# Optimization experiments

Hardware: AMD Instinct MI355X
Metric: run time of the kernel (lower is better)

## Reference

```python
import jax, jax.numpy as jnp
import numpy as np

N_EMBD = 2048
N_HEAD = 16
KV_GROUP = 4
HEAD_DIM = N_EMBD // N_HEAD          # 128
N_KV = N_HEAD // KV_GROUP            # 4
KV_DIM = N_KV * HEAD_DIM             # 512
B, T = 2, 2048
ROPE_THETA = 1000000.0


def setup_inputs() -> dict:
    key = jax.random.key(0)
    k0, k1, k2 = jax.random.split(key, 3)
    x = jax.random.normal(k0, (B, T, N_EMBD), dtype=jnp.float32)
    # weights stored (in, out); matches torch Linear math up to a transpose of random init
    W_attn = jax.random.normal(k1, (N_EMBD, N_EMBD + 2 * KV_DIM), dtype=jnp.float32) * 0.02
    b_attn = jnp.zeros((N_EMBD + 2 * KV_DIM,), dtype=jnp.float32)
    W_proj = jax.random.normal(k2, (N_EMBD, N_EMBD), dtype=jnp.float32) * 0.02
    # realistic RoPE frequencies (Qwen-style theta)
    inv_freq = 1.0 / (ROPE_THETA ** (np.arange(0, HEAD_DIM, 2, dtype=np.float64) / HEAD_DIM))
    ang = np.outer(np.arange(T, dtype=np.float64), inv_freq)  # (T, HEAD_DIM//2)
    freqs_cos = jnp.asarray(np.cos(ang), dtype=jnp.float32)
    freqs_sin = jnp.asarray(np.sin(ang), dtype=jnp.float32)
    return {"x": x, "W_attn": W_attn, "b_attn": b_attn, "W_proj": W_proj,
            "freqs_cos": freqs_cos, "freqs_sin": freqs_sin}


def _rope_expand(x, cos, sin, kv_group):
    # x: (B, T, n_kv, hd); complex rotate interleaved pairs, then expand to n_kv*kv_group heads
    Bx, Tx, nh, hd = x.shape
    xf = x.astype(jnp.float32).reshape(Bx, Tx, nh, hd // 2, 2)
    a, b = xf[..., 0], xf[..., 1]
    c = cos[None, :, None, :]  # (1, T, 1, hd//2)
    s = sin[None, :, None, :]
    yr = a * c - b * s
    yi = a * s + b * c
    y = jnp.stack([yr, yi], axis=-1).reshape(Bx, Tx, nh, hd)
    y = jnp.broadcast_to(y[:, :, :, None, :], (Bx, Tx, nh, kv_group, hd))
    return y.reshape(Bx, Tx, nh * kv_group, hd).astype(x.dtype)


def reference(x, W_attn, b_attn, W_proj, freqs_cos, freqs_sin):
    Bx, Tx, E = x.shape
    hd = 2 * freqs_cos.shape[-1]
    n_q = E // hd
    kv_dim = (W_attn.shape[1] - E) // 2
    n_kv = kv_dim // hd
    g = n_q // n_kv

    qkv = x @ W_attn + b_attn  # (B, T, E + 2*kv_dim)
    q = qkv[..., :E].reshape(Bx, Tx, n_q, hd).transpose(0, 2, 1, 3)          # bhtd
    k = qkv[..., E:E + kv_dim].reshape(Bx, Tx, n_kv, hd)
    v = qkv[..., E + kv_dim:].reshape(Bx, Tx, n_kv, hd)
    # faithful to source: RoPE on K AND V (not Q), then GQA expand
    k = _rope_expand(k, freqs_cos, freqs_sin, g).transpose(0, 2, 1, 3)       # bhtd
    v = _rope_expand(v, freqs_cos, freqs_sin, g).transpose(0, 2, 1, 3)       # bhtd

    scale = 1.0 / jnp.sqrt(jnp.asarray(hd, dtype=x.dtype))
    scores = jnp.einsum('bhqd,bhkd->bhqk', q, k) * scale                     # (B, H, T, T)
    causal = jnp.tril(jnp.ones((Tx, Tx), dtype=bool))
    scores = jnp.where(causal, scores, jnp.asarray(-jnp.inf, scores.dtype))
    attn = jax.nn.softmax(scores, axis=-1)
    y = jnp.einsum('bhqk,bhkd->bhqd', attn, v)
    y = y.transpose(0, 2, 1, 3).reshape(Bx, Tx, E)
    return y @ W_proj  # c_proj, no bias
```

## Files before the change

kernel.cpp:

```cpp
#include <hip/hip_runtime.h>
#include <cstdint>
#include <cstddef>

#define T_SEQ 2048
#define B_SZ  2
#define EMB   2048
#define NH    16
#define NKV   4
#define HD    128
#define KVD   512
#define QKVN  3072
#define MROWS (B_SZ*T_SEQ)

typedef __bf16 bf16x8 __attribute__((ext_vector_type(8)));
typedef float  f32x4  __attribute__((ext_vector_type(4)));
typedef short  s16x8  __attribute__((ext_vector_type(8)));
typedef unsigned short u16;

__device__ __forceinline__ u16 f2b(float f) {
  uint32_t u = __builtin_bit_cast(uint32_t, f);
  u += 0x7fffu + ((u >> 16) & 1u);
  return (u16)(u >> 16);
}
__device__ __forceinline__ float b2f(u16 h) {
  return __builtin_bit_cast(float, (uint32_t)h << 16);
}
__device__ __forceinline__ bf16x8 ld_bf8(const u16* p) {
  return __builtin_bit_cast(bf16x8, *(const s16x8*)p);
}
__device__ __forceinline__ void glds16(const void* g, void* l) {
  __builtin_amdgcn_global_load_lds((const __attribute__((address_space(1))) void*)g,
                                   (__attribute__((address_space(3))) void*)l, 16, 0, 0);
}

__global__ void cvt_x_kernel(const float4* __restrict__ x, ushort4* __restrict__ xb, int n4) {
  int i = blockIdx.x*blockDim.x + threadIdx.x;
  if (i >= n4) return;
  float4 v = x[i];
  ushort4 o;
  o.x = f2b(v.x); o.y = f2b(v.y); o.z = f2b(v.z); o.w = f2b(v.w);
  xb[i] = o;
}

__global__ void transpose_w_kernel(const float* __restrict__ in, u16* __restrict__ out,
                                   int R, int C) {
  __shared__ float tile[32][33];
  int c0 = blockIdx.x*32, r0 = blockIdx.y*32;
  int tx = threadIdx.x, ty = threadIdx.y;
#pragma unroll
  for (int i = 0; i < 32; i += 8)
    tile[ty+i][tx] = in[(size_t)(r0+ty+i)*C + c0+tx];
  __syncthreads();
#pragma unroll
  for (int i = 0; i < 32; i += 8)
    out[(size_t)(c0+ty+i)*R + r0+tx] = f2b(tile[tx][ty+i]);
}

template<bool BF16_OUT>
__global__ __launch_bounds__(256) void gemm_kernel(const u16* __restrict__ A,
        const u16* __restrict__ Bt, const float* __restrict__ bias,
        void* __restrict__ Cout, int M, int N, int K) {
  __shared__ u16 As[128*64];
  __shared__ u16 Bs[128*64];
  const int tid = threadIdx.x;
  const int w = tid >> 6, lane = tid & 63;
  const int quad = lane >> 4, lc = lane & 15;
  const int m0 = blockIdx.y*128, n0 = blockIdx.x*128;
  const int wm = (w >> 1)*64, wn = (w & 1)*64;
  f32x4 acc[4][4] = {};
  int xoff[2];
#pragma unroll
  for (int ks = 0; ks < 2; ++ks) xoff[ks] = ((ks*4 + quad) ^ (lc & 7))*8;
  int srow[4], spos[4];
#pragma unroll
  for (int r = 0; r < 4; ++r) {
    int c = r*256 + tid;
    srow[r] = c >> 3;
    spos[r] = ((c & 7) ^ (srow[r] & 7))*8;
  }
  for (int k0 = 0; k0 < K; k0 += 64) {
    __syncthreads();
#pragma unroll
    for (int r = 0; r < 4; ++r) {
      glds16(A  + (size_t)(m0+srow[r])*K + k0 + spos[r], As + (size_t)(r*256 + w*64)*8);
      glds16(Bt + (size_t)(n0+srow[r])*K + k0 + spos[r], Bs + (size_t)(r*256 + w*64)*8);
    }
    __syncthreads();
#pragma unroll
    for (int ks = 0; ks < 2; ++ks) {
      bf16x8 af[4], bfr[4];
#pragma unroll
      for (int i = 0; i < 4; ++i) af[i]  = ld_bf8(As + (wm + i*16 + lc)*64 + xoff[ks]);
#pragma unroll
      for (int j = 0; j < 4; ++j) bfr[j] = ld_bf8(Bs + (wn + j*16 + lc)*64 + xoff[ks]);
#pragma unroll
      for (int i = 0; i < 4; ++i)
#pragma unroll
        for (int j = 0; j < 4; ++j)
          acc[i][j] = __builtin_amdgcn_mfma_f32_16x16x32_bf16(af[i], bfr[j], acc[i][j], 0, 0, 0);
    }
  }
#pragma unroll
  for (int j = 0; j < 4; ++j) {
    int col = n0 + wn + j*16 + lc;
    float bv = BF16_OUT ? bias[col] : 0.0f;
#pragma unroll
    for (int i = 0; i < 4; ++i) {
      int rowb = m0 + wm + i*16 + quad*4;
#pragma unroll
      for (int r = 0; r < 4; ++r) {
        float v = acc[i][j][r] + bv;
        if (BF16_OUT) ((u16*)Cout)[(size_t)(rowb+r)*N + col] = f2b(v);
        else          ((float*)Cout)[(size_t)(rowb+r)*N + col] = v;
      }
    }
  }
}

__global__ void rope_kernel(const u16* __restrict__ qkv, const float* __restrict__ fc,
                            const float* __restrict__ fs, u16* __restrict__ kout,
                            u16* __restrict__ vout) {
  int tid = threadIdx.x;
  int row = blockIdx.x;
  int i = tid & 63, kv = tid >> 6;
  int t = row & (T_SEQ-1);
  const u16* p = qkv + (size_t)row*QKVN + EMB + kv*HD + 2*i;
  float ka = b2f(p[0]),   kb = b2f(p[1]);
  float va = b2f(p[KVD]), vb = b2f(p[KVD+1]);
  float c = fc[t*64+i], s = fs[t*64+i];
  size_t ob = (size_t)row*KVD + kv*HD + 2*i;
  kout[ob]   = f2b(ka*c - kb*s);
  kout[ob+1] = f2b(ka*s + kb*c);
  vout[ob]   = f2b(va*c - vb*s);
  vout[ob+1] = f2b(va*s + vb*c);
}

__global__ void transpose_v_kernel(const u16* __restrict__ vb, u16* __restrict__ vtb) {
  __shared__ u16 tile[32][33];
  int bkv = blockIdx.z;
  int b = bkv >> 2, kv = bkv & 3;
  int d0 = blockIdx.y*32, t0 = blockIdx.x*32;
  int tx = threadIdx.x, ty = threadIdx.y;
#pragma unroll
  for (int i = 0; i < 32; i += 8)
    tile[ty+i][tx] = vb[(size_t)(b*T_SEQ + t0+ty+i)*KVD + kv*HD + d0 + tx];
  __syncthreads();
#pragma unroll
  for (int i = 0; i < 32; i += 8)
    vtb[(size_t)(bkv*HD + d0+ty+i)*T_SEQ + t0 + tx] = tile[tx][ty+i];
}

__global__ __launch_bounds__(256, 3) void flash_kernel(const u16* __restrict__ qkv,
    const u16* __restrict__ kb, const u16* __restrict__ vtb, u16* __restrict__ yb) {
  constexpr int PP = 72;
  __shared__ u16 Ks[64*128];
  __shared__ u16 Vs[128*64];
  __shared__ u16 Ps[4][16*PP];
  const int tid = threadIdx.x;
  const int w = tid >> 6, lane = tid & 63;
  const int quad = lane >> 4, lc = lane & 15;
  const int bkv = blockIdx.x & 7;
  const int r_  = blockIdx.x >> 3;
  const int b = bkv >> 2, kv = bkv & 3;
  const int h = kv*4 + w;
  const int qbase = (127 - r_)*16;

  bf16x8 qf[4];
  {
    const u16* qp = qkv + (size_t)(b*T_SEQ + qbase + lc)*QKVN + h*HD + quad*8;
#pragma unroll
    for (int ks = 0; ks < 4; ++ks) qf[ks] = ld_bf8(qp + ks*32);
  }

  f32x4 o[8] = {};
  float rs[4] = {0.f, 0.f, 0.f, 0.f};
  const u16* kbase = kb  + (size_t)b*T_SEQ*KVD + kv*HD;
  const u16* vbase = vtb + (size_t)bkv*HD*T_SEQ;
  const int nk = qbase + 16;
  const float cs = 0.08838834764831845f * 1.4426950408889634f;
  u16* pw = Ps[w];

  int koff[4], voff[2];
#pragma unroll
  for (int ks = 0; ks < 4; ++ks) koff[ks] = lc*128 + (((ks*4 + quad) ^ lc)*8);
#pragma unroll
  for (int ks = 0; ks < 2; ++ks) voff[ks] = lc*64 + (((ks*4 + quad) ^ (lc & 7))*8);

  for (int k0 = 0; k0 < nk; k0 += 64) {
    __syncthreads();
#pragma unroll
    for (int rr = 0; rr < 4; ++rr) {
      int krow = (rr*4 + w)*4 + (lane >> 4);
      int ccg  = (lane & 15) ^ (krow & 15);
      glds16(kbase + (size_t)(k0 + krow)*KVD + ccg*8, Ks + (size_t)(rr*4 + w)*512);
    }
#pragma unroll
    for (int rr = 0; rr < 4; ++rr) {
      int vrow = (rr*4 + w)*8 + (lane >> 3);
      int ccg  = (lane & 7) ^ (vrow & 7);
      glds16(vbase + (size_t)vrow*T_SEQ + k0 + ccg*8, Vs + (size_t)(rr*4 + w)*512);
    }
    __syncthreads();

    f32x4 sc[4] = {};
#pragma unroll
    for (int nt = 0; nt < 4; ++nt)
#pragma unroll
      for (int ks = 0; ks < 4; ++ks) {
        bf16x8 kf = ld_bf8(Ks + nt*16*128 + koff[ks]);
        sc[nt] = __builtin_amdgcn_mfma_f32_16x16x32_bf16(qf[ks], kf, sc[nt], 0, 0, 0);
      }

    if (k0 + 63 > qbase) {
#pragma unroll
      for (int nt = 0; nt < 4; ++nt) {
        int key = k0 + nt*16 + lc;
        int qrow = qbase + quad*4;
#pragma unroll
        for (int r = 0; r < 4; ++r) {
          float p = (key <= qrow + r) ? exp2f(sc[nt][r]*cs) : 0.0f;
          rs[r] += p;
          pw[(quad*4 + r)*PP + nt*16 + lc] = f2b(p);
        }
      }
    } else {
#pragma unroll
      for (int nt = 0; nt < 4; ++nt)
#pragma unroll
        for (int r = 0; r < 4; ++r) {
          float p = exp2f(sc[nt][r]*cs);
          rs[r] += p;
          pw[(quad*4 + r)*PP + nt*16 + lc] = f2b(p);
        }
    }

    bf16x8 pa[2];
#pragma unroll
    for (int ks = 0; ks < 2; ++ks)
      pa[ks] = ld_bf8(pw + lc*PP + ks*32 + quad*8);

#pragma unroll
    for (int j = 0; j < 8; ++j)
#pragma unroll
      for (int ks = 0; ks < 2; ++ks) {
        bf16x8 vf = ld_bf8(Vs + j*16*64 + voff[ks]);
        o[j] = __builtin_amdgcn_mfma_f32_16x16x32_bf16(pa[ks], vf, o[j], 0, 0, 0);
      }
  }

#pragma unroll
  for (int r = 0; r < 4; ++r) {
    float v = rs[r];
#pragma unroll
    for (int off2 = 8; off2 >= 1; off2 >>= 1)
      v += __shfl_xor(v, off2);
    float inv = 1.0f / v;
    size_t orow = (size_t)(b*T_SEQ + qbase + quad*4 + r)*EMB + h*HD;
#pragma unroll
    for (int j = 0; j < 8; ++j)
      yb[orow + j*16 + lc] = f2b(o[j][r]*inv);
  }
}

extern "C" void kernel_launch(void* const* d_in, const int* in_sizes, int n_in,
                              void* d_out, int out_size, void* d_ws, size_t ws_size,
                              hipStream_t stream) {
  const float* x      = (const float*)d_in[0];
  const float* W_attn = (const float*)d_in[1];
  const float* b_attn = (const float*)d_in[2];
  const float* W_proj = (const float*)d_in[3];
  const float* fc     = (const float*)d_in[4];
  const float* fs     = (const float*)d_in[5];

  u16* ws   = (u16*)d_ws;
  u16* xb   = ws;
  u16* WaT  = xb   + (size_t)MROWS*EMB;
  u16* qkv  = WaT  + (size_t)QKVN*EMB;
  u16* kbuf = qkv  + (size_t)MROWS*QKVN;
  u16* vb   = kbuf + (size_t)MROWS*KVD;
  u16* vtb  = vb   + (size_t)MROWS*KVD;
  u16* WpT  = WaT;
  u16* yb   = xb;
  float* out = (float*)d_out;

  cvt_x_kernel<<<(MROWS*EMB/4 + 255)/256, 256, 0, stream>>>(
      (const float4*)x, (ushort4*)xb, MROWS*EMB/4);
  transpose_w_kernel<<<dim3(QKVN/32, EMB/32), dim3(32, 8), 0, stream>>>(
      W_attn, WaT, EMB, QKVN);
  gemm_kernel<true><<<dim3(QKVN/128, MROWS/128), 256, 0, stream>>>(
      xb, WaT, b_attn, qkv, MROWS, QKVN, EMB);
  rope_kernel<<<MROWS, 256, 0, stream>>>(qkv, fc, fs, kbuf, vb);
  transpose_v_kernel<<<dim3(T_SEQ/32, HD/32, B_SZ*NKV), dim3(32, 8), 0, stream>>>(vb, vtb);
  transpose_w_kernel<<<dim3(EMB/32, EMB/32), dim3(32, 8), 0, stream>>>(
      W_proj, WpT, EMB, EMB);
  flash_kernel<<<dim3(B_SZ*NKV*(T_SEQ/16)), 256, 0, stream>>>(qkv, kbuf, vtb, yb);
  gemm_kernel<false><<<dim3(EMB/128, MROWS/128), 256, 0, stream>>>(
      yb, WpT, nullptr, out, MROWS, EMB, EMB);
}
```

Measured before the change: 307.0 us.

## Replace GEMM with 256x256 double-buffered, phase-scheduled MFMA pipeline

Both projection GEMMs move to a 512-thread kernel with 256x256 output tiles and double-buffered LDS. Global-to-LDS loads of the next K tile are interleaved with MFMA phases, using explicit barriers, waitcnt and setprio scheduling. The aim is to hide memory latency and raise data reuse per block. In exchange there are far fewer blocks (192 and 128), which can leave CUs idle, and register pressure is higher.

```diff
diff --git a/kernel.cpp b/kernel.cpp
--- a/kernel.cpp
+++ b/kernel.cpp
@@ -57,56 +57,136 @@
 }
 
 template<bool BF16_OUT>
-__global__ __launch_bounds__(256) void gemm_kernel(const u16* __restrict__ A,
+__global__ __launch_bounds__(512, 2) void gemm256_kernel(const u16* __restrict__ A,
         const u16* __restrict__ Bt, const float* __restrict__ bias,
         void* __restrict__ Cout, int M, int N, int K) {
-  __shared__ u16 As[128*64];
-  __shared__ u16 Bs[128*64];
+  __shared__ u16 As[2][16384];
+  __shared__ u16 Bs[2][16384];
   const int tid = threadIdx.x;
   const int w = tid >> 6, lane = tid & 63;
   const int quad = lane >> 4, lc = lane & 15;
-  const int m0 = blockIdx.y*128, n0 = blockIdx.x*128;
-  const int wm = (w >> 1)*64, wn = (w & 1)*64;
-  f32x4 acc[4][4] = {};
-  int xoff[2];
-#pragma unroll
-  for (int ks = 0; ks < 2; ++ks) xoff[ks] = ((ks*4 + quad) ^ (lc & 7))*8;
-  int srow[4], spos[4];
-#pragma unroll
-  for (int r = 0; r < 4; ++r) {
-    int c = r*256 + tid;
-    srow[r] = c >> 3;
-    spos[r] = ((c & 7) ^ (srow[r] & 7))*8;
-  }
-  for (int k0 = 0; k0 < K; k0 += 64) {
-    __syncthreads();
-#pragma unroll
-    for (int r = 0; r < 4; ++r) {
-      glds16(A  + (size_t)(m0+srow[r])*K + k0 + spos[r], As + (size_t)(r*256 + w*64)*8);
-      glds16(Bt + (size_t)(n0+srow[r])*K + k0 + spos[r], Bs + (size_t)(r*256 + w*64)*8);
-    }
-    __syncthreads();
-#pragma unroll
-    for (int ks = 0; ks < 2; ++ks) {
-      bf16x8 af[4], bfr[4];
-#pragma unroll
-      for (int i = 0; i < 4; ++i) af[i]  = ld_bf8(As + (wm + i*16 + lc)*64 + xoff[ks]);
-#pragma unroll
-      for (int j = 0; j < 4; ++j) bfr[j] = ld_bf8(Bs + (wn + j*16 + lc)*64 + xoff[ks]);
-#pragma unroll
-      for (int i = 0; i < 4; ++i)
-#pragma unroll
-        for (int j = 0; j < 4; ++j)
-          acc[i][j] = __builtin_amdgcn_mfma_f32_16x16x32_bf16(af[i], bfr[j], acc[i][j], 0, 0, 0);
-    }
-  }
+  const int wr = w >> 2, wc = w & 3;
+  const int m0 = blockIdx.y*256, n0 = blockIdx.x*256;
+
+  f32x4 acc[8][4] = {};
+  bf16x8 af[4][2], bfv[4][2];
+
+  int aoff[2];
+#pragma unroll
+  for (int ks = 0; ks < 2; ++ks) aoff[ks] = ((ks*4 + quad) ^ (lc & 7))*8;
+  const int arow = (wr*128 + lc)*64;
+  const int brow = (wc*64  + lc)*64;
+
+  const int r0 = tid >> 3,          p0 = (tid & 7) ^ (r0 & 7);
+  const int r1 = (tid + 512) >> 3,  p1 = (tid & 7) ^ (r1 & 7);
+  const u16* sa0 = A  + (size_t)(m0 + r0)*K + p0*8;
+  const u16* sa1 = A  + (size_t)(m0 + r1)*K + p1*8;
+  const u16* sb0 = Bt + (size_t)(n0 + r0)*K + p0*8;
+  const u16* sb1 = Bt + (size_t)(n0 + r1)*K + p1*8;
+  const int wch = w*512;
+
+#define STAGE_A(bf_, h_, t_) do { \
+    glds16(sa0 + (size_t)(h_)*128*K + (t_)*64, &As[bf_][(h_)*8192 + wch]); \
+    glds16(sa1 + (size_t)(h_)*128*K + (t_)*64, &As[bf_][(h_)*8192 + 4096 + wch]); \
+  } while (0)
+#define STAGE_B(bf_, h_, t_) do { \
+    glds16(sb0 + (size_t)(h_)*128*K + (t_)*64, &Bs[bf_][(h_)*8192 + wch]); \
+    glds16(sb1 + (size_t)(h_)*128*K + (t_)*64, &Bs[bf_][(h_)*8192 + 4096 + wch]); \
+  } while (0)
+#define LDA03(S) do { _Pragma("unroll") for (int i = 0; i < 4; ++i) { \
+    af[i][0] = ld_bf8((S) + arow + i*1024 + aoff[0]); \
+    af[i][1] = ld_bf8((S) + arow + i*1024 + aoff[1]); } } while (0)
+#define LDA47(S) do { _Pragma("unroll") for (int i = 0; i < 4; ++i) { \
+    af[i][0] = ld_bf8((S) + arow + 4096 + i*1024 + aoff[0]); \
+    af[i][1] = ld_bf8((S) + arow + 4096 + i*1024 + aoff[1]); } } while (0)
+#define LDB01(S) do { _Pragma("unroll") for (int j = 0; j < 2; ++j) { \
+    bfv[j][0] = ld_bf8((S) + brow + j*1024 + aoff[0]); \
+    bfv[j][1] = ld_bf8((S) + brow + j*1024 + aoff[1]); } } while (0)
+#define LDB23(S) do { _Pragma("unroll") for (int j = 2; j < 4; ++j) { \
+    bfv[j][0] = ld_bf8((S) + brow + j*1024 + aoff[0]); \
+    bfv[j][1] = ld_bf8((S) + brow + j*1024 + aoff[1]); } } while (0)
+#define QUAD(ib_, jb_) do { _Pragma("unroll") for (int ks = 0; ks < 2; ++ks) \
+    _Pragma("unroll") for (int i = 0; i < 4; ++i) \
+    _Pragma("unroll") for (int j = 0; j < 2; ++j) \
+      acc[(ib_)+i][(jb_)+j] = __builtin_amdgcn_mfma_f32_16x16x32_bf16( \
+          af[i][ks], bfv[(jb_)+j][ks], acc[(ib_)+i][(jb_)+j], 0, 0, 0); } while (0)
+#define BARX()  __builtin_amdgcn_s_barrier()
+#define SCHB()  __builtin_amdgcn_sched_barrier(0)
+#define VMCNT(n_) do { asm volatile("s_waitcnt vmcnt(" #n_ ")" ::: "memory"); SCHB(); } while (0)
+#define MFMAPH(ib_, jb_) do { BARX(); \
+    asm volatile("s_waitcnt lgkmcnt(0)" ::: "memory"); SCHB(); \
+    __builtin_amdgcn_s_setprio(1); QUAD(ib_, jb_); __builtin_amdgcn_s_setprio(0); \
+  } while (0)
+
+  const int NT = K >> 6;
+  STAGE_A(0, 0, 0); STAGE_A(0, 1, 0); STAGE_B(0, 0, 0); STAGE_B(0, 1, 0);
+  STAGE_B(1, 0, 1); STAGE_B(1, 1, 1);
+  VMCNT(4);
+  BARX(); SCHB();
+
+  for (int t0 = 0; t0 < NT-2; t0 += 2) {
+    const int t1 = t0 + 1;
+    const u16 *a0 = As[0], *b0 = Bs[0], *a1 = As[1], *b1 = Bs[1];
+    LDA03(a0); LDB01(b0); STAGE_A(1, 0, t1);
+    MFMAPH(0, 0); BARX();
+    LDB23(b0); STAGE_A(1, 1, t1);
+    MFMAPH(0, 2); BARX();
+    LDA47(a0); STAGE_B(0, 0, t0+2);
+    MFMAPH(4, 0); BARX();
+    STAGE_B(0, 1, t0+2);
+    MFMAPH(4, 2);
+    VMCNT(4);
+    BARX(); SCHB();
+    LDA03(a1); LDB01(b1); STAGE_A(0, 0, t0+2);
+    MFMAPH(0, 0); BARX();
+    LDB23(b1); STAGE_A(0, 1, t0+2);
+    MFMAPH(0, 2); BARX();
+    LDA47(a1); STAGE_B(1, 0, t1+2);
+    MFMAPH(4, 0); BARX();
+    STAGE_B(1, 1, t1+2);
+    MFMAPH(4, 2);
+    VMCNT(4);
+    BARX(); SCHB();
+  }
+  {
+    const u16 *a0 = As[0], *b0 = Bs[0], *a1 = As[1], *b1 = Bs[1];
+    LDA03(a0); LDB01(b0); STAGE_A(1, 0, NT-1);
+    MFMAPH(0, 0); BARX();
+    LDB23(b0); STAGE_A(1, 1, NT-1);
+    MFMAPH(0, 2); BARX();
+    LDA47(a0);
+    MFMAPH(4, 0); BARX();
+    MFMAPH(4, 2);
+    VMCNT(0);
+    BARX(); SCHB();
+    LDA03(a1); LDB01(b1);
+    MFMAPH(0, 0); BARX();
+    LDB23(b1);
+    MFMAPH(0, 2); BARX();
+    LDA47(a1);
+    MFMAPH(4, 0); BARX();
+    MFMAPH(4, 2);
+  }
+
+#undef STAGE_A
+#undef STAGE_B
+#undef LDA03
+#undef LDA47
+#undef LDB01
+#undef LDB23
+#undef QUAD
+#undef BARX
+#undef SCHB
+#undef VMCNT
+#undef MFMAPH
+
 #pragma unroll
   for (int j = 0; j < 4; ++j) {
-    int col = n0 + wn + j*16 + lc;
+    int col = n0 + wc*64 + j*16 + lc;
     float bv = BF16_OUT ? bias[col] : 0.0f;
 #pragma unroll
-    for (int i = 0; i < 4; ++i) {
-      int rowb = m0 + wm + i*16 + quad*4;
+    for (int i = 0; i < 8; ++i) {
+      int rowb = m0 + wr*128 + i*16 + quad*4;
 #pragma unroll
       for (int r = 0; r < 4; ++r) {
         float v = acc[i][j][r] + bv;
@@ -287,13 +367,13 @@
       (const float4*)x, (ushort4*)xb, MROWS*EMB/4);
   transpose_w_kernel<<<dim3(QKVN/32, EMB/32), dim3(32, 8), 0, stream>>>(
       W_attn, WaT, EMB, QKVN);
-  gemm_kernel<true><<<dim3(QKVN/128, MROWS/128), 256, 0, stream>>>(
+  gemm256_kernel<true><<<dim3(QKVN/256, MROWS/256), 512, 0, stream>>>(
       xb, WaT, b_attn, qkv, MROWS, QKVN, EMB);
   rope_kernel<<<MROWS, 256, 0, stream>>>(qkv, fc, fs, kbuf, vb);
   transpose_v_kernel<<<dim3(T_SEQ/32, HD/32, B_SZ*NKV), dim3(32, 8), 0, stream>>>(vb, vtb);
   transpose_w_kernel<<<dim3(EMB/32, EMB/32), dim3(32, 8), 0, stream>>>(
       W_proj, WpT, EMB, EMB);
   flash_kernel<<<dim3(B_SZ*NKV*(T_SEQ/16)), 256, 0, stream>>>(qkv, kbuf, vtb, yb);
-  gemm_kernel<false><<<dim3(EMB/128, MROWS/128), 256, 0, stream>>>(
+  gemm256_kernel<false><<<dim3(EMB/256, MROWS/256), 512, 0, stream>>>(
       yb, WpT, nullptr, out, MROWS, EMB, EMB);
 }
```

After: 309.3 us. No clear change (+0.8%).

## Rewrite GEMM with double-buffered LDS pipeline, larger tiles, and block swizzle

Applied to the files above, without the earlier changes.

Replaces the single-buffered 128x128 GEMM with a templated 512-thread kernel that uses 256-row tiles and double-buffered LDS. Global-to-LDS loads for the next K tile are interleaved with MFMA phases under explicit vmcnt waits, barriers and setprio. A swizzled block index is also added to improve L2 reuse. In exchange it needs much more LDS and more registers, and the hand-written wait counts and barriers are fragile.

```diff
diff --git a/kernel.cpp b/kernel.cpp
--- a/kernel.cpp
+++ b/kernel.cpp
@@ -32,6 +32,12 @@
   __builtin_amdgcn_global_load_lds((const __attribute__((address_space(1))) void*)g,
                                    (__attribute__((address_space(3))) void*)l, 16, 0, 0);
 }
+template<int N> __device__ __forceinline__ void waitv() {
+  if constexpr (N == 0) asm volatile("s_waitcnt vmcnt(0)" ::: "memory");
+  else if constexpr (N == 2) asm volatile("s_waitcnt vmcnt(2)" ::: "memory");
+  else if constexpr (N == 3) asm volatile("s_waitcnt vmcnt(3)" ::: "memory");
+  __builtin_amdgcn_sched_barrier(0);
+}
 
 __global__ void cvt_x_kernel(const float4* __restrict__ x, ushort4* __restrict__ xb, int n4) {
   int i = blockIdx.x*blockDim.x + threadIdx.x;
@@ -56,57 +62,128 @@
     out[(size_t)(c0+ty+i)*R + r0+tx] = f2b(tile[tx][ty+i]);
 }
 
-template<bool BF16_OUT>
-__global__ __launch_bounds__(256) void gemm_kernel(const u16* __restrict__ A,
+template<int BN, int WGN, int MF, int NF, int NF1, int SB, int SB1, int VMC, bool BF16_OUT>
+__global__ __launch_bounds__(512, 2) void gemm_kernel(const u16* __restrict__ A,
         const u16* __restrict__ Bt, const float* __restrict__ bias,
         void* __restrict__ Cout, int M, int N, int K) {
-  __shared__ u16 As[128*64];
-  __shared__ u16 Bs[128*64];
+  constexpr int MF2 = MF/2;
+  __shared__ u16 As[2][256*64];
+  __shared__ u16 Bs[2][BN*64];
   const int tid = threadIdx.x;
   const int w = tid >> 6, lane = tid & 63;
   const int quad = lane >> 4, lc = lane & 15;
-  const int m0 = blockIdx.y*128, n0 = blockIdx.x*128;
-  const int wm = (w >> 1)*64, wn = (w & 1)*64;
-  f32x4 acc[4][4] = {};
+  const int wrow = w / WGN, wcol = w % WGN;
+  const int gx = gridDim.x;
+  const int lin = blockIdx.y*gx + blockIdx.x;
+  const int swz = (lin & 7)*32 + (lin >> 3);
+  const int m0 = (swz / gx)*256, n0 = (swz % gx)*BN;
+
+  f32x4 acc[MF][NF] = {};
+  bf16x8 af[MF2][2], bfv[NF][2];
+
   int xoff[2];
 #pragma unroll
   for (int ks = 0; ks < 2; ++ks) xoff[ks] = ((ks*4 + quad) ^ (lc & 7))*8;
-  int srow[4], spos[4];
-#pragma unroll
-  for (int r = 0; r < 4; ++r) {
-    int c = r*256 + tid;
-    srow[r] = c >> 3;
-    spos[r] = ((c & 7) ^ (srow[r] & 7))*8;
-  }
-  for (int k0 = 0; k0 < K; k0 += 64) {
-    __syncthreads();
-#pragma unroll
-    for (int r = 0; r < 4; ++r) {
-      glds16(A  + (size_t)(m0+srow[r])*K + k0 + spos[r], As + (size_t)(r*256 + w*64)*8);
-      glds16(Bt + (size_t)(n0+srow[r])*K + k0 + spos[r], Bs + (size_t)(r*256 + w*64)*8);
-    }
-    __syncthreads();
-#pragma unroll
-    for (int ks = 0; ks < 2; ++ks) {
-      bf16x8 af[4], bfr[4];
-#pragma unroll
-      for (int i = 0; i < 4; ++i) af[i]  = ld_bf8(As + (wm + i*16 + lc)*64 + xoff[ks]);
-#pragma unroll
-      for (int j = 0; j < 4; ++j) bfr[j] = ld_bf8(Bs + (wn + j*16 + lc)*64 + xoff[ks]);
-#pragma unroll
-      for (int i = 0; i < 4; ++i)
-#pragma unroll
-        for (int j = 0; j < 4; ++j)
-          acc[i][j] = __builtin_amdgcn_mfma_f32_16x16x32_bf16(af[i], bfr[j], acc[i][j], 0, 0, 0);
-    }
-  }
-#pragma unroll
-  for (int j = 0; j < 4; ++j) {
-    int col = n0 + wn + j*16 + lc;
+  const int arow0 = (wrow*MF*16 + lc)*64;
+  const int brow0 = (wcol*NF*16 + lc)*64;
+
+  const int srb  = tid >> 3;
+  const int spos = (tid & 7) ^ (srb & 7);
+  const u16* sAp = A  + (size_t)(m0 + srb)*K + spos*8;
+  const u16* sBp = Bt + (size_t)(n0 + srb)*K + spos*8;
+
+#define STAGE_A(bf_, t_, h_) do { \
+    glds16(sAp + (size_t)((h_)*2  )*64*K + (size_t)(t_)*64, &As[bf_][((h_)*2  )*4096 + w*512]); \
+    glds16(sAp + (size_t)((h_)*2+1)*64*K + (size_t)(t_)*64, &As[bf_][((h_)*2+1)*4096 + w*512]); \
+  } while (0)
+#define STAGE_B(bf_, t_, p_) do { \
+    _Pragma("unroll") for (int r = (p_) ? SB1 : 0; r < ((p_) ? SB : SB1); ++r) \
+      glds16(sBp + (size_t)r*64*K + (size_t)(t_)*64, &Bs[bf_][r*4096 + w*512]); \
+  } while (0)
+#define LDAH(S_, h_) do { _Pragma("unroll") for (int i = 0; i < MF2; ++i) { \
+    af[i][0] = ld_bf8((S_) + arow0 + ((h_)*MF2 + i)*1024 + xoff[0]); \
+    af[i][1] = ld_bf8((S_) + arow0 + ((h_)*MF2 + i)*1024 + xoff[1]); } } while (0)
+#define LDBG(S_, g_) do { _Pragma("unroll") for (int j = (g_) ? NF1 : 0; j < ((g_) ? NF : NF1); ++j) { \
+    bfv[j][0] = ld_bf8((S_) + brow0 + j*1024 + xoff[0]); \
+    bfv[j][1] = ld_bf8((S_) + brow0 + j*1024 + xoff[1]); } } while (0)
+#define CL(h_, g_) do { _Pragma("unroll") for (int ks = 0; ks < 2; ++ks) \
+    _Pragma("unroll") for (int i = 0; i < MF2; ++i) \
+    _Pragma("unroll") for (int j = (g_) ? NF1 : 0; j < ((g_) ? NF : NF1); ++j) \
+      acc[(h_)*MF2+i][j] = __builtin_amdgcn_mfma_f32_16x16x32_bf16( \
+          af[i][ks], bfv[j][ks], acc[(h_)*MF2+i][j], 0, 0, 0); } while (0)
+#define BARX()  __builtin_amdgcn_s_barrier()
+#define SCHB()  __builtin_amdgcn_sched_barrier(0)
+#define MFMAPH(h_, g_) do { BARX(); \
+    asm volatile("s_waitcnt lgkmcnt(0)" ::: "memory"); SCHB(); \
+    __builtin_amdgcn_s_setprio(1); CL(h_, g_); __builtin_amdgcn_s_setprio(0); \
+  } while (0)
+
+  const int NT = K >> 6;
+  STAGE_B(0, 0, 0); STAGE_B(0, 0, 1);
+  STAGE_A(0, 0, 0); STAGE_A(0, 0, 1);
+  STAGE_B(1, 1, 0); STAGE_B(1, 1, 1);
+  waitv<VMC>();
+  BARX(); SCHB();
+
+  for (int t0 = 0; t0 < NT-2; t0 += 2) {
+    const u16 *a0 = As[0], *b0 = Bs[0], *a1 = As[1], *b1 = Bs[1];
+    LDAH(a0, 0); LDBG(b0, 0); STAGE_A(1, t0+1, 0);
+    MFMAPH(0, 0); BARX();
+    LDBG(b0, 1); STAGE_A(1, t0+1, 1);
+    MFMAPH(0, 1); BARX();
+    LDAH(a0, 1); STAGE_B(0, t0+2, 0);
+    MFMAPH(1, 0); BARX();
+    STAGE_B(0, t0+2, 1);
+    MFMAPH(1, 1);
+    waitv<VMC>();
+    BARX(); SCHB();
+    LDAH(a1, 0); LDBG(b1, 0); STAGE_A(0, t0+2, 0);
+    MFMAPH(0, 0); BARX();
+    LDBG(b1, 1); STAGE_A(0, t0+2, 1);
+    MFMAPH(0, 1); BARX();
+    LDAH(a1, 1); STAGE_B(1, t0+3, 0);
+    MFMAPH(1, 0); BARX();
+    STAGE_B(1, t0+3, 1);
+    MFMAPH(1, 1);
+    waitv<VMC>();
+    BARX(); SCHB();
+  }
+  {
+    const u16 *a0 = As[0], *b0 = Bs[0], *a1 = As[1], *b1 = Bs[1];
+    LDAH(a0, 0); LDBG(b0, 0); STAGE_A(1, NT-1, 0);
+    MFMAPH(0, 0); BARX();
+    LDBG(b0, 1); STAGE_A(1, NT-1, 1);
+    MFMAPH(0, 1); BARX();
+    LDAH(a0, 1);
+    MFMAPH(1, 0); BARX();
+    MFMAPH(1, 1);
+    waitv<0>();
+    BARX(); SCHB();
+    LDAH(a1, 0); LDBG(b1, 0);
+    MFMAPH(0, 0); BARX();
+    LDBG(b1, 1);
+    MFMAPH(0, 1); BARX();
+    LDAH(a1, 1);
+    MFMAPH(1, 0); BARX();
+    MFMAPH(1, 1);
+  }
+
+#undef STAGE_A
+#undef STAGE_B
+#undef LDAH
+#undef LDBG
+#undef CL
+#undef BARX
+#undef SCHB
+#undef MFMAPH
+
+#pragma unroll
+  for (int j = 0; j < NF; ++j) {
+    int col = n0 + wcol*NF*16 + j*16 + lc;
     float bv = BF16_OUT ? bias[col] : 0.0f;
 #pragma unroll
-    for (int i = 0; i < 4; ++i) {
-      int rowb = m0 + wm + i*16 + quad*4;
+    for (int i = 0; i < MF; ++i) {
+      int rowb = m0 + wrow*MF*16 + i*16 + quad*4;
 #pragma unroll
       for (int r = 0; r < 4; ++r) {
         float v = acc[i][j][r] + bv;
@@ -287,13 +364,15 @@
       (const float4*)x, (ushort4*)xb, MROWS*EMB/4);
   transpose_w_kernel<<<dim3(QKVN/32, EMB/32), dim3(32, 8), 0, stream>>>(
       W_attn, WaT, EMB, QKVN);
-  gemm_kernel<true><<<dim3(QKVN/128, MROWS/128), 256, 0, stream>>>(
+  gemm_kernel<192, 4, 8, 3, 2, 3, 2, 3, true>
+      <<<dim3(QKVN/192, MROWS/256), 512, 0, stream>>>(
       xb, WaT, b_attn, qkv, MROWS, QKVN, EMB);
   rope_kernel<<<MROWS, 256, 0, stream>>>(qkv, fc, fs, kbuf, vb);
   transpose_v_kernel<<<dim3(T_SEQ/32, HD/32, B_SZ*NKV), dim3(32, 8), 0, stream>>>(vb, vtb);
   transpose_w_kernel<<<dim3(EMB/32, EMB/32), dim3(32, 8), 0, stream>>>(
       W_proj, WpT, EMB, EMB);
   flash_kernel<<<dim3(B_SZ*NKV*(T_SEQ/16)), 256, 0, stream>>>(qkv, kbuf, vtb, yb);
-  gemm_kernel<false><<<dim3(EMB/128, MROWS/128), 256, 0, stream>>>(
+  gemm_kernel<128, 2, 4, 4, 2, 2, 1, 2, false>
+      <<<dim3(EMB/128, MROWS/256), 512, 0, stream>>>(
       yb, WpT, nullptr, out, MROWS, EMB, EMB);
 }
```

Measured after the change: 285.3 us. 1.08x faster.
